# Performance work log

Measured on AMD Instinct MI355X. Metric: run time of the kernel, lower is better.

## Reference

```python
import jax, jax.numpy as jnp
import numpy as np

TOPK = 4          # config.top_prob_values
NBINS = 32        # config.max_num_bins -> bins per corner = NBINS+1 = 33
HID = 64          # config.lqe_hidden_dim
B, L = 64, 4096


def setup_inputs() -> dict:
    key = jax.random.key(0)
    k1, k2, k3, k4 = jax.random.split(key, 4)
    in_dim = 4 * (TOPK + 1)  # 20
    scores = jax.random.normal(k1, (B, L, 1), dtype=jnp.float32)
    pred_corners = jax.random.normal(k2, (B, L, 4 * (NBINS + 1)), dtype=jnp.float32)
    # Deimv2MLP (DFineMLP) with num_layers=2: Linear(20,64) -> relu -> Linear(64,1)
    w1 = jax.random.normal(k3, (in_dim, HID), dtype=jnp.float32) / np.sqrt(in_dim)
    b1 = jnp.zeros((HID,), dtype=jnp.float32)
    w2 = jax.random.normal(k4, (HID, 1), dtype=jnp.float32) / np.sqrt(HID)
    b2 = jnp.zeros((1,), dtype=jnp.float32)
    return {"scores": scores, "pred_corners": pred_corners,
            "w1": w1, "b1": b1, "w2": w2, "b2": b2}


def reference(scores, pred_corners, w1, b1, w2, b2):
    b, l, _ = pred_corners.shape
    # softmax over bins per corner: (B, L, 4, NBINS+1)
    prob = jax.nn.softmax(pred_corners.reshape(b, l, 4, NBINS + 1), axis=-1)
    prob_topk, _ = jax.lax.top_k(prob, TOPK)                     # (B, L, 4, TOPK)
    stat = jnp.concatenate([prob_topk,
                            prob_topk.mean(axis=-1, keepdims=True)], axis=-1)
    stat = stat.reshape(b, l, 4 * (TOPK + 1))                    # (B, L, 20)
    h = jax.nn.relu(stat @ w1 + b1)                              # (B, L, 64)
    quality_score = h @ w2 + b2                                  # (B, L, 1)
    return scores + quality_score
```

## Files before the change

### kernel.cpp

```cpp
#include <hip/hip_runtime.h>


#define THREADS 256

typedef float f32x4 __attribute__((ext_vector_type(4), aligned(4)));

__device__ __forceinline__ void sort4d(float& a, float& b, float& c, float& d) {
    float t;
    t = fmaxf(a, b); b = fminf(a, b); a = t;
    t = fmaxf(c, d); d = fminf(c, d); c = t;
    t = fmaxf(a, c); c = fminf(a, c); a = t;
    t = fmaxf(b, d); d = fminf(b, d); b = t;
    t = fmaxf(b, c); c = fminf(b, c); b = t;
}
__device__ __forceinline__ void ins4(float& a, float& b, float& c, float& d,
                                     float x) {
    float t;
    t = fmaxf(a, x); x = fminf(a, x); a = t;
    t = fmaxf(b, x); x = fminf(b, x); b = t;
    t = fmaxf(c, x); x = fminf(c, x); c = t;
    d = fmaxf(d, x);
}
__device__ __forceinline__ void merge4(float& a0, float& a1, float& a2,
                                       float& a3, float b0, float b1,
                                       float b2, float b3) {
    a0 = fmaxf(a0, b3);
    a1 = fmaxf(a1, b2);
    a2 = fmaxf(a2, b1);
    a3 = fmaxf(a3, b0);
    sort4d(a0, a1, a2, a3);
}

__global__ __launch_bounds__(THREADS, 4)
void lqe_kernel(const float* __restrict__ scores,
                const float* __restrict__ pc,
                const float* __restrict__ w1,
                const float* __restrict__ b1,
                const float* __restrict__ w2,
                const float* __restrict__ b2,
                float* __restrict__ out)
{
    __shared__ float sm_stat[4][64 * 21];

    const int tid = threadIdx.x;
    const int wv = tid >> 6;
    const int l  = tid & 63;
    float* const statS = sm_stat[wv];

    const long long waveRowBase = (long long)blockIdx.x * 256 + wv * 64;
    const float myScore = scores[waveRowBase + l];

    #pragma unroll
    for (int s = 0; s < 4; ++s) {
        const float* base =
            pc + (waveRowBase + s * 16 + (l >> 2)) * 132 + (l & 3) * 33;

        float x[33];
        #pragma unroll
        for (int i = 0; i < 8; ++i) {
            f32x4 v = *(const f32x4*)(base + i * 4);
            x[4*i+0] = v.x; x[4*i+1] = v.y; x[4*i+2] = v.z; x[4*i+3] = v.w;
        }
        x[32] = base[32];

        float a0 = x[0],  a1 = x[1],  a2 = x[2],  a3 = x[3];
        float c0 = x[8],  c1 = x[9],  c2 = x[10], c3 = x[11];
        float d0 = x[16], d1 = x[17], d2 = x[18], d3 = x[19];
        float e0 = x[24], e1 = x[25], e2 = x[26], e3 = x[27];
        sort4d(a0, a1, a2, a3);
        sort4d(c0, c1, c2, c3);
        sort4d(d0, d1, d2, d3);
        sort4d(e0, e1, e2, e3);
        #pragma unroll
        for (int k = 0; k < 4; ++k) {
            ins4(a0, a1, a2, a3, x[4 + k]);
            ins4(c0, c1, c2, c3, x[12 + k]);
            ins4(d0, d1, d2, d3, x[20 + k]);
            ins4(e0, e1, e2, e3, x[28 + k]);
        }
        ins4(e0, e1, e2, e3, x[32]);
        merge4(a0, a1, a2, a3, c0, c1, c2, c3);
        merge4(d0, d1, d2, d3, e0, e1, e2, e3);
        merge4(a0, a1, a2, a3, d0, d1, d2, d3);
        const float t0 = a0, t1 = a1, t2 = a2, t3 = a3;

        float sa = 0.f, sb = 0.f, sc = 0.f, sd = 0.f;
        #pragma unroll
        for (int k = 0; k < 32; k += 4) {
            sa += __expf(x[k + 0] - t0);
            sb += __expf(x[k + 1] - t0);
            sc += __expf(x[k + 2] - t0);
            sd += __expf(x[k + 3] - t0);
        }
        sa += __expf(x[32] - t0);
        const float inv = 1.0f / ((sa + sb) + (sc + sd));
        const float p0 = inv;
        const float p1 = __expf(t1 - t0) * inv;
        const float p2 = __expf(t2 - t0) * inv;
        const float p3 = __expf(t3 - t0) * inv;
        const float pm = 0.25f * (p0 + p1 + p2 + p3);

        float* sd_ = statS + (s * 16 + (l >> 2)) * 21 + (l & 3) * 5;
        sd_[0] = p0; sd_[1] = p1; sd_[2] = p2; sd_[3] = p3; sd_[4] = pm;
    }

    float st[20];
    #pragma unroll
    for (int k = 0; k < 20; ++k) st[k] = statS[l * 21 + k];

    float acc0 = 0.f, acc1 = 0.f, acc2 = 0.f, acc3 = 0.f;
    #pragma unroll
    for (int jc = 0; jc < 4; ++jc) {
        float h[16];
        #pragma unroll
        for (int j = 0; j < 16; ++j) h[j] = b1[jc * 16 + j];
        #pragma unroll
        for (int k = 0; k < 20; ++k) {
            #pragma unroll
            for (int j = 0; j < 16; ++j)
                h[j] = fmaf(st[k], w1[k * 64 + jc * 16 + j], h[j]);
        }
        #pragma unroll
        for (int j = 0; j < 16; j += 4) {
            acc0 = fmaf(fmaxf(h[j + 0], 0.f), w2[jc * 16 + j + 0], acc0);
            acc1 = fmaf(fmaxf(h[j + 1], 0.f), w2[jc * 16 + j + 1], acc1);
            acc2 = fmaf(fmaxf(h[j + 2], 0.f), w2[jc * 16 + j + 2], acc2);
            acc3 = fmaf(fmaxf(h[j + 3], 0.f), w2[jc * 16 + j + 3], acc3);
        }
    }

    out[waveRowBase + l] = myScore + ((acc0 + acc1) + (acc2 + acc3)) + b2[0];
}

extern "C" void kernel_launch(void* const* d_in, const int* in_sizes, int n_in,
                              void* d_out, int out_size, void* d_ws, size_t ws_size,
                              hipStream_t stream) {
    const float* scores = (const float*)d_in[0];
    const float* pc     = (const float*)d_in[1];
    const float* w1     = (const float*)d_in[2];
    const float* b1     = (const float*)d_in[3];
    const float* w2     = (const float*)d_in[4];
    const float* b2     = (const float*)d_in[5];
    float* out = (float*)d_out;

    const int rows = out_size;
    const int blocks = rows / 256;
    lqe_kernel<<<blocks, THREADS, 0, stream>>>(scores, pc, w1, b1, w2, b2, out);
}
```

Before: 40.23 us.

## Stage input rows through LDS with coalesced loads and split MLP across waves

Result: faster. 32.66 us (-18.8%).

```diff
diff --git a/kernel.cpp b/kernel.cpp
--- a/kernel.cpp
+++ b/kernel.cpp
@@ -2,8 +2,9 @@
 
 
 #define THREADS 256
+#define ROWS 64
 
-typedef float f32x4 __attribute__((ext_vector_type(4), aligned(4)));
+typedef float f32x4 __attribute__((ext_vector_type(4), aligned(16)));
 
 __device__ __forceinline__ void sort4d(float& a, float& b, float& c, float& d) {
     float t;
@@ -40,28 +41,26 @@
                 const float* __restrict__ b2,
                 float* __restrict__ out)
 {
-    __shared__ float sm_stat[4][64 * 21];
+    __shared__ float sm_stage[ROWS * 132];
+    __shared__ float sm_stat[ROWS * 21];
 
-    const int tid = threadIdx.x;
-    const int wv = tid >> 6;
-    const int l  = tid & 63;
-    float* const statS = sm_stat[wv];
+    const int t = threadIdx.x;
+    const long long rowBase = (long long)blockIdx.x * ROWS;
 
-    const long long waveRowBase = (long long)blockIdx.x * 256 + wv * 64;
-    const float myScore = scores[waveRowBase + l];
+    {
+        const f32x4* __restrict__ src = (const f32x4*)(pc + rowBase * 132);
+        f32x4* dst = (f32x4*)sm_stage;
+        #pragma unroll
+        for (int i = 0; i < 8; ++i) dst[t + i * 256] = src[t + i * 256];
+        if (t < 64) dst[2048 + t] = src[2048 + t];
+    }
+    __syncthreads();
 
-    #pragma unroll
-    for (int s = 0; s < 4; ++s) {
-        const float* base =
-            pc + (waveRowBase + s * 16 + (l >> 2)) * 132 + (l & 3) * 33;
-
+    {
+        const float* v = sm_stage + t * 33;
         float x[33];
         #pragma unroll
-        for (int i = 0; i < 8; ++i) {
-            f32x4 v = *(const f32x4*)(base + i * 4);
-            x[4*i+0] = v.x; x[4*i+1] = v.y; x[4*i+2] = v.z; x[4*i+3] = v.w;
-        }
-        x[32] = base[32];
+        for (int k = 0; k < 33; ++k) x[k] = v[k];
 
         float a0 = x[0],  a1 = x[1],  a2 = x[2],  a3 = x[3];
         float c0 = x[8],  c1 = x[9],  c2 = x[10], c3 = x[11];
@@ -100,36 +99,48 @@
         const float p3 = __expf(t3 - t0) * inv;
         const float pm = 0.25f * (p0 + p1 + p2 + p3);
 
-        float* sd_ = statS + (s * 16 + (l >> 2)) * 21 + (l & 3) * 5;
+        float* sd_ = sm_stat + (t >> 2) * 21 + (t & 3) * 5;
         sd_[0] = p0; sd_[1] = p1; sd_[2] = p2; sd_[3] = p3; sd_[4] = pm;
     }
+    __syncthreads();
 
-    float st[20];
-    #pragma unroll
-    for (int k = 0; k < 20; ++k) st[k] = statS[l * 21 + k];
+    {
+        const int l  = t & 63;
+        const int wv = __builtin_amdgcn_readfirstlane(t >> 6);
+        const float* __restrict__ w1s = w1 + wv * 16;
+        const float* __restrict__ w2s = w2 + wv * 16;
+        const float* __restrict__ b1s = b1 + wv * 16;
 
-    float acc0 = 0.f, acc1 = 0.f, acc2 = 0.f, acc3 = 0.f;
-    #pragma unroll
-    for (int jc = 0; jc < 4; ++jc) {
+        float st[20];
+        #pragma unroll
+        for (int k = 0; k < 20; ++k) st[k] = sm_stat[l * 21 + k];
+
         float h[16];
         #pragma unroll
-        for (int j = 0; j < 16; ++j) h[j] = b1[jc * 16 + j];
+        for (int j = 0; j < 16; ++j) h[j] = b1s[j];
         #pragma unroll
         for (int k = 0; k < 20; ++k) {
             #pragma unroll
             for (int j = 0; j < 16; ++j)
-                h[j] = fmaf(st[k], w1[k * 64 + jc * 16 + j], h[j]);
+                h[j] = fmaf(st[k], w1s[k * 64 + j], h[j]);
         }
+        float acc0 = 0.f, acc1 = 0.f, acc2 = 0.f, acc3 = 0.f;
         #pragma unroll
         for (int j = 0; j < 16; j += 4) {
-            acc0 = fmaf(fmaxf(h[j + 0], 0.f), w2[jc * 16 + j + 0], acc0);
-            acc1 = fmaf(fmaxf(h[j + 1], 0.f), w2[jc * 16 + j + 1], acc1);
-            acc2 = fmaf(fmaxf(h[j + 2], 0.f), w2[jc * 16 + j + 2], acc2);
-            acc3 = fmaf(fmaxf(h[j + 3], 0.f), w2[jc * 16 + j + 3], acc3);
+            acc0 = fmaf(fmaxf(h[j + 0], 0.f), w2s[j + 0], acc0);
+            acc1 = fmaf(fmaxf(h[j + 1], 0.f), w2s[j + 1], acc1);
+            acc2 = fmaf(fmaxf(h[j + 2], 0.f), w2s[j + 2], acc2);
+            acc3 = fmaf(fmaxf(h[j + 3], 0.f), w2s[j + 3], acc3);
         }
+        sm_stage[wv * 64 + l] = (acc0 + acc1) + (acc2 + acc3);
     }
+    __syncthreads();
 
-    out[waveRowBase + l] = myScore + ((acc0 + acc1) + (acc2 + acc3)) + b2[0];
+    if (t < 64) {
+        const float r = (sm_stage[t] + sm_stage[64 + t]) +
+                        (sm_stage[128 + t] + sm_stage[192 + t]);
+        out[rowBase + t] = scores[rowBase + t] + r + b2[0];
+    }
 }
 
 extern "C" void kernel_launch(void* const* d_in, const int* in_sizes, int n_in,
@@ -144,6 +155,6 @@
     float* out = (float*)d_out;
 
     const int rows = out_size;
-    const int blocks = rows / 256;
+    const int blocks = rows / ROWS;
     lqe_kernel<<<blocks, THREADS, 0, stream>>>(scores, pc, w1, b1, w2, b2, out);
 }
```
